# Kernel tuning notes

Measured on AMD Instinct MI355X. Metric: run time of the kernel, lower is better.

The kernel has to match this reference:

```python
import jax, jax.numpy as jnp
import numpy as np

HIDDEN_DIM = 64
VOCAB_SIZE = 64
NUM_SLOTS = 64
B, L = 256, 4096
EPS = 1e-5


def setup_inputs() -> dict:
    key = jax.random.key(0)
    ks = jax.random.split(key, 8)
    s = 0.02
    return {
        "seq": jax.random.randint(ks[0], (B, L), 0, VOCAB_SIZE),
        "embed": jax.random.normal(ks[1], (VOCAB_SIZE, HIDDEN_DIM), jnp.float32) * s,
        "W1": jax.random.normal(ks[2], (HIDDEN_DIM, 2 * HIDDEN_DIM), jnp.float32) * s,
        "b1": jnp.zeros((2 * HIDDEN_DIM,), jnp.float32),
        "W2": jax.random.normal(ks[3], (2 * HIDDEN_DIM, HIDDEN_DIM), jnp.float32) * s,
        "b2": jnp.zeros((HIDDEN_DIM,), jnp.float32),
        "gamma": jnp.ones((HIDDEN_DIM,), jnp.float32),
        "beta": jnp.zeros((HIDDEN_DIM,), jnp.float32),
        "Wq": jax.random.normal(ks[4], (HIDDEN_DIM, HIDDEN_DIM), jnp.float32) * s,
        "bq": jnp.zeros((HIDDEN_DIM,), jnp.float32),
        "Wo": jax.random.normal(ks[5], (HIDDEN_DIM, VOCAB_SIZE), jnp.float32) * s,
        "bo": jnp.zeros((VOCAB_SIZE,), jnp.float32),
    }


def reference(seq, embed, W1, b1, W2, b2, gamma, beta, Wq, bq, Wo, bo):
    # Encoder: embed -> FF residual -> LayerNorm
    e = embed[seq]                                   # [B, L, H]
    ff = jax.nn.relu(e @ W1 + b1) @ W2 + b2          # [B, L, H]
    h = e + ff
    mu = jnp.mean(h, axis=-1, keepdims=True)
    var = jnp.mean(jnp.square(h - mu), axis=-1, keepdims=True)
    hs = (h - mu) * jax.lax.rsqrt(var + EPS) * gamma + beta  # [B, L, H]

    # Top-k gating over content token norms
    content = hs[:, :-3, :]                          # [B, L-3, H]
    gate_scores = jnp.linalg.norm(content, axis=-1)  # [B, L-3]
    _, idx = jax.lax.top_k(gate_scores, NUM_SLOTS)   # [B, k], k == num_slots (L-3 >= k)
    slots = jnp.take_along_axis(content, idx[:, :, None], axis=1)  # [B, k, H]

    # Tiny single-query attention over gathered slots
    q = hs[:, -1, :] @ Wq + bq                       # [B, H]
    scores = jnp.einsum("bh,bkh->bk", q, slots) / jnp.sqrt(jnp.float32(HIDDEN_DIM))
    attn = jax.nn.softmax(scores, axis=-1)           # [B, k]
    ctx = jnp.einsum("bk,bkh->bh", attn, slots)      # [B, H]
    return ctx @ Wo + bo                             # [B, VOCAB]
```

## Files before the change

kernel.cpp:

```cpp
#include <hip/hip_runtime.h>
#include <math.h>

#define EPS 1e-5f

__global__ __launch_bounds__(256) void build_table(
    const float* __restrict__ embed,
    const float* __restrict__ W1, const float* __restrict__ b1,
    const float* __restrict__ W2, const float* __restrict__ b2,
    const float* __restrict__ gamma, const float* __restrict__ beta,
    float* __restrict__ wsf)
{
    __shared__ float W1s[64][128];
    __shared__ float W2s[128][64];
    __shared__ float e[64];
    __shared__ float Up[2][128];
    __shared__ float U[128];
    __shared__ float Hp[4][64];

    const int tid = threadIdx.x;
    const int t   = blockIdx.x;

    #pragma unroll
    for (int i = 0; i < 8; ++i) {
        reinterpret_cast<float4*>(&W1s[0][0])[tid + 256 * i] =
            reinterpret_cast<const float4*>(W1)[tid + 256 * i];
        reinterpret_cast<float4*>(&W2s[0][0])[tid + 256 * i] =
            reinterpret_cast<const float4*>(W2)[tid + 256 * i];
    }
    if (tid < 64) e[tid] = embed[t * 64 + tid];
    __syncthreads();

    {
        int j = tid & 127, h = tid >> 7;
        int k0 = h << 5;
        float acc = 0.f;
        #pragma unroll 8
        for (int k = 0; k < 32; ++k)
            acc = fmaf(e[k0 + k], W1s[k0 + k][j], acc);
        Up[h][j] = acc;
    }
    __syncthreads();
    if (tid < 128) U[tid] = fmaxf(b1[tid] + Up[0][tid] + Up[1][tid], 0.f);
    __syncthreads();

    {
        int j = tid & 63, qd = tid >> 6;
        int k0 = qd << 5;
        float acc = 0.f;
        #pragma unroll 8
        for (int k = 0; k < 32; ++k)
            acc = fmaf(U[k0 + k], W2s[k0 + k][j], acc);
        Hp[qd][j] = acc;
    }
    __syncthreads();

    if (tid < 64) {
        float h = e[tid] + b2[tid] + Hp[0][tid] + Hp[1][tid] + Hp[2][tid] + Hp[3][tid];
        float s = h;
        #pragma unroll
        for (int off = 1; off < 64; off <<= 1) s += __shfl_xor(s, off);
        float mu = s * (1.f / 64.f);
        float d = h - mu;
        float v = d * d;
        #pragma unroll
        for (int off = 1; off < 64; off <<= 1) v += __shfl_xor(v, off);
        float rstd = rsqrtf(v * (1.f / 64.f) + EPS);
        float hs = d * rstd * gamma[tid] + beta[tid];
        wsf[t * 64 + tid] = hs;
        float ss = hs * hs;
        #pragma unroll
        for (int off = 1; off < 64; off <<= 1) ss += __shfl_xor(ss, off);
        if (tid == 0) wsf[4096 + t] = sqrtf(ss);
    }
}

__global__ __launch_bounds__(256) void slot_epilogue(
    const int* __restrict__ seq,
    const float* __restrict__ Wq, const float* __restrict__ bq,
    const float* __restrict__ Wo, const float* __restrict__ bo,
    const float* __restrict__ wsf,
    float* __restrict__ out)
{
    __shared__ float HS[64][65];
    __shared__ int   hist[4][64];
    __shared__ float qv[64];
    __shared__ int   tlast_s;

    const int tid = threadIdx.x;
    const int wv  = tid >> 6;
    const int ln  = tid & 63;
    const int b   = blockIdx.x;
    const int* row = seq + b * 4096;

    hist[wv][ln] = 0;

    float wcol[64];
    float bias = 0.f, sc_r = 0.f;
    if (wv == 0) {
        #pragma unroll
        for (int k = 0; k < 64; ++k) wcol[k] = Wo[k * 64 + ln];
        bias = bo[ln];
        sc_r = wsf[4096 + ln];
    } else if (wv == 1) {
        #pragma unroll
        for (int k = 0; k < 64; ++k) wcol[k] = Wq[k * 64 + ln];
        bias = bq[ln];
    }

    #pragma unroll
    for (int i = 0; i < 4; ++i) {
        int idx4 = tid + 256 * i;
        float4 v = reinterpret_cast<const float4*>(wsf)[idx4];
        int t  = idx4 >> 4;
        int j0 = (idx4 & 15) << 2;
        HS[t][j0] = v.x; HS[t][j0 + 1] = v.y; HS[t][j0 + 2] = v.z; HS[t][j0 + 3] = v.w;
    }

    #pragma unroll
    for (int i = 0; i < 4; ++i) {
        int idx = tid + 256 * i;
        if (idx < 1023) {
            int4 v = reinterpret_cast<const int4*>(row)[idx];
            atomicAdd(&hist[wv][v.x], 1);
            atomicAdd(&hist[wv][v.y], 1);
            atomicAdd(&hist[wv][v.z], 1);
            atomicAdd(&hist[wv][v.w], 1);
        }
    }
    if (tid == 0) {
        atomicAdd(&hist[0][row[4092]], 1);
        tlast_s = row[4095];
    }
    __syncthreads();

    int cnt_i = 0;
    if (wv == 0) {
        int h = hist[0][ln] + hist[1][ln] + hist[2][ln] + hist[3][ln];
        float my = sc_r;
        int S = 0;
        for (int t2 = 0; t2 < 64; ++t2) {
            float s2 = __shfl(sc_r, t2);
            int   h2 = __shfl(h, t2);
            bool before = (s2 > my) || (s2 == my && t2 < ln);
            if (before) S += h2;
        }
        int rem = 64 - S;
        rem = rem < 0 ? 0 : rem;
        cnt_i = h < rem ? h : rem;
    } else if (wv == 1) {
        int tl = tlast_s;
        float acc = bias;
        #pragma unroll
        for (int k = 0; k < 64; ++k)
            acc = fmaf(HS[tl][k], wcol[k], acc);
        qv[ln] = acc;
    }
    __syncthreads();

    if (wv == 0) {
        float acc = 0.f;
        #pragma unroll 8
        for (int k = 0; k < 64; ++k)
            acc = fmaf(qv[k], HS[ln][k], acc);
        float logit = acc * 0.125f;
        float lm = (cnt_i > 0) ? logit : -1e30f;
        #pragma unroll
        for (int off = 1; off < 64; off <<= 1) lm = fmaxf(lm, __shfl_xor(lm, off));
        float wvv = (cnt_i > 0) ? (float)cnt_i * __expf(logit - lm) : 0.f;
        float z = wvv;
        #pragma unroll
        for (int off = 1; off < 64; off <<= 1) z += __shfl_xor(z, off);
        float w_reg = wvv / z;

        float cacc = 0.f;
        #pragma unroll 8
        for (int t2 = 0; t2 < 64; ++t2)
            cacc = fmaf(__shfl(w_reg, t2), HS[t2][ln], cacc);

        float oacc = bias;
        #pragma unroll
        for (int k = 0; k < 64; ++k)
            oacc = fmaf(__shfl(cacc, k), wcol[k], oacc);
        out[b * 64 + ln] = oacc;
    }
}

extern "C" void kernel_launch(void* const* d_in, const int* in_sizes, int n_in,
                              void* d_out, int out_size, void* d_ws, size_t ws_size,
                              hipStream_t stream) {
    const int*   seq   = (const int*)d_in[0];
    const float* embed = (const float*)d_in[1];
    const float* W1    = (const float*)d_in[2];
    const float* b1    = (const float*)d_in[3];
    const float* W2    = (const float*)d_in[4];
    const float* b2    = (const float*)d_in[5];
    const float* gamma = (const float*)d_in[6];
    const float* beta  = (const float*)d_in[7];
    const float* Wq    = (const float*)d_in[8];
    const float* bq    = (const float*)d_in[9];
    const float* Wo    = (const float*)d_in[10];
    const float* bo    = (const float*)d_in[11];
    float* out = (float*)d_out;
    float* wsf = (float*)d_ws;
    (void)in_sizes; (void)n_in; (void)out_size; (void)ws_size;

    build_table<<<64, 256, 0, stream>>>(embed, W1, b1, W2, b2, gamma, beta, wsf);
    slot_epilogue<<<256, 256, 0, stream>>>(seq, Wq, bq, Wo, bo, wsf, out);
}
```

Baseline: 16.98 us.

## Move per-row token histogram into first kernel to overlap with table build

The token histogram and last-token lookup over each sequence row now run in extra blocks of the first kernel, alongside the 64 table-building blocks, instead of inside the epilogue kernel. Per-row counts and the last-token index are written to workspace, and the epilogue only reads them. The aim is to hide the 4 MB sequence read behind the small table build, which uses few CUs, and to shorten the dependent second kernel. The cost is extra workspace traffic, plus one uniform launch that reserves the table path's large shared memory even in histogram blocks, which may reduce occupancy.

```diff
diff --git a/kernel.cpp b/kernel.cpp
--- a/kernel.cpp
+++ b/kernel.cpp
@@ -3,108 +3,141 @@
 
 #define EPS 1e-5f
 
-__global__ __launch_bounds__(256) void build_table(
+
+__global__ __launch_bounds__(256) void table_and_hist(
+    const int* __restrict__ seq,
     const float* __restrict__ embed,
     const float* __restrict__ W1, const float* __restrict__ b1,
     const float* __restrict__ W2, const float* __restrict__ b2,
     const float* __restrict__ gamma, const float* __restrict__ beta,
-    float* __restrict__ wsf)
+    float* __restrict__ wsf, int* __restrict__ wsi_hist,
+    int* __restrict__ wsi_tlast)
 {
-    __shared__ float W1s[64][128];
-    __shared__ float W2s[128][64];
-    __shared__ float e[64];
-    __shared__ float Up[2][128];
-    __shared__ float U[128];
-    __shared__ float Hp[4][64];
-
     const int tid = threadIdx.x;
-    const int t   = blockIdx.x;
-
-    #pragma unroll
-    for (int i = 0; i < 8; ++i) {
-        reinterpret_cast<float4*>(&W1s[0][0])[tid + 256 * i] =
-            reinterpret_cast<const float4*>(W1)[tid + 256 * i];
-        reinterpret_cast<float4*>(&W2s[0][0])[tid + 256 * i] =
-            reinterpret_cast<const float4*>(W2)[tid + 256 * i];
-    }
-    if (tid < 64) e[tid] = embed[t * 64 + tid];
-    __syncthreads();
-
-    {
-        int j = tid & 127, h = tid >> 7;
-        int k0 = h << 5;
-        float acc = 0.f;
-        #pragma unroll 8
-        for (int k = 0; k < 32; ++k)
-            acc = fmaf(e[k0 + k], W1s[k0 + k][j], acc);
-        Up[h][j] = acc;
-    }
-    __syncthreads();
-    if (tid < 128) U[tid] = fmaxf(b1[tid] + Up[0][tid] + Up[1][tid], 0.f);
-    __syncthreads();
-
-    {
-        int j = tid & 63, qd = tid >> 6;
-        int k0 = qd << 5;
-        float acc = 0.f;
-        #pragma unroll 8
-        for (int k = 0; k < 32; ++k)
-            acc = fmaf(U[k0 + k], W2s[k0 + k][j], acc);
-        Hp[qd][j] = acc;
-    }
-    __syncthreads();
-
-    if (tid < 64) {
-        float h = e[tid] + b2[tid] + Hp[0][tid] + Hp[1][tid] + Hp[2][tid] + Hp[3][tid];
-        float s = h;
-        #pragma unroll
-        for (int off = 1; off < 64; off <<= 1) s += __shfl_xor(s, off);
-        float mu = s * (1.f / 64.f);
-        float d = h - mu;
-        float v = d * d;
-        #pragma unroll
-        for (int off = 1; off < 64; off <<= 1) v += __shfl_xor(v, off);
-        float rstd = rsqrtf(v * (1.f / 64.f) + EPS);
-        float hs = d * rstd * gamma[tid] + beta[tid];
-        wsf[t * 64 + tid] = hs;
-        float ss = hs * hs;
-        #pragma unroll
-        for (int off = 1; off < 64; off <<= 1) ss += __shfl_xor(ss, off);
-        if (tid == 0) wsf[4096 + t] = sqrtf(ss);
+
+    if (blockIdx.x < 64) {
+        __shared__ float W1s[64][128];
+        __shared__ float W2s[128][64];
+        __shared__ float e[64];
+        __shared__ float Up[2][128];
+        __shared__ float U[128];
+        __shared__ float Hp[4][64];
+
+        const int t = blockIdx.x;
+
+        #pragma unroll
+        for (int i = 0; i < 8; ++i) {
+            reinterpret_cast<float4*>(&W1s[0][0])[tid + 256 * i] =
+                reinterpret_cast<const float4*>(W1)[tid + 256 * i];
+            reinterpret_cast<float4*>(&W2s[0][0])[tid + 256 * i] =
+                reinterpret_cast<const float4*>(W2)[tid + 256 * i];
+        }
+        if (tid < 64) e[tid] = embed[t * 64 + tid];
+        __syncthreads();
+
+        {
+            int j = tid & 127, h = tid >> 7;
+            int k0 = h << 5;
+            float acc = 0.f;
+            #pragma unroll 8
+            for (int k = 0; k < 32; ++k)
+                acc = fmaf(e[k0 + k], W1s[k0 + k][j], acc);
+            Up[h][j] = acc;
+        }
+        __syncthreads();
+        if (tid < 128) U[tid] = fmaxf(b1[tid] + Up[0][tid] + Up[1][tid], 0.f);
+        __syncthreads();
+
+        {
+            int j = tid & 63, qd = tid >> 6;
+            int k0 = qd << 5;
+            float acc = 0.f;
+            #pragma unroll 8
+            for (int k = 0; k < 32; ++k)
+                acc = fmaf(U[k0 + k], W2s[k0 + k][j], acc);
+            Hp[qd][j] = acc;
+        }
+        __syncthreads();
+
+        if (tid < 64) {
+            float h = e[tid] + b2[tid] + Hp[0][tid] + Hp[1][tid] + Hp[2][tid] + Hp[3][tid];
+            float s = h;
+            #pragma unroll
+            for (int off = 1; off < 64; off <<= 1) s += __shfl_xor(s, off);
+            float mu = s * (1.f / 64.f);
+            float d = h - mu;
+            float v = d * d;
+            #pragma unroll
+            for (int off = 1; off < 64; off <<= 1) v += __shfl_xor(v, off);
+            float rstd = rsqrtf(v * (1.f / 64.f) + EPS);
+            float hs = d * rstd * gamma[tid] + beta[tid];
+            wsf[t * 64 + tid] = hs;
+            float ss = hs * hs;
+            #pragma unroll
+            for (int off = 1; off < 64; off <<= 1) ss += __shfl_xor(ss, off);
+            if (tid == 0) wsf[4096 + t] = sqrtf(ss);
+        }
+    } else {
+        __shared__ int hist[4][64];
+        const int b = blockIdx.x - 64;
+        const int wv = tid >> 6, ln = tid & 63;
+        const int* row = seq + b * 4096;
+
+        hist[wv][ln] = 0;
+        __syncthreads();
+
+        #pragma unroll
+        for (int i = 0; i < 4; ++i) {
+            int idx = tid + 256 * i;
+            if (idx < 1023) {
+                int4 v = reinterpret_cast<const int4*>(row)[idx];
+                atomicAdd(&hist[wv][v.x], 1);
+                atomicAdd(&hist[wv][v.y], 1);
+                atomicAdd(&hist[wv][v.z], 1);
+                atomicAdd(&hist[wv][v.w], 1);
+            }
+        }
+        if (tid == 0) {
+            atomicAdd(&hist[0][row[4092]], 1);
+            wsi_tlast[b] = row[4095];
+        }
+        __syncthreads();
+
+        if (tid < 64)
+            wsi_hist[b * 64 + tid] =
+                hist[0][tid] + hist[1][tid] + hist[2][tid] + hist[3][tid];
     }
 }
 
 __global__ __launch_bounds__(256) void slot_epilogue(
-    const int* __restrict__ seq,
     const float* __restrict__ Wq, const float* __restrict__ bq,
     const float* __restrict__ Wo, const float* __restrict__ bo,
-    const float* __restrict__ wsf,
+    const float* __restrict__ wsf, const int* __restrict__ wsi_hist,
+    const int* __restrict__ wsi_tlast,
     float* __restrict__ out)
 {
     __shared__ float HS[64][65];
-    __shared__ int   hist[4][64];
     __shared__ float qv[64];
-    __shared__ int   tlast_s;
 
     const int tid = threadIdx.x;
     const int wv  = tid >> 6;
     const int ln  = tid & 63;
     const int b   = blockIdx.x;
-    const int* row = seq + b * 4096;
-
-    hist[wv][ln] = 0;
 
     float wcol[64];
     float bias = 0.f, sc_r = 0.f;
+    int h = 0, tl = 0;
     if (wv == 0) {
         #pragma unroll
         for (int k = 0; k < 64; ++k) wcol[k] = Wo[k * 64 + ln];
         bias = bo[ln];
         sc_r = wsf[4096 + ln];
+        h    = wsi_hist[b * 64 + ln];
     } else if (wv == 1) {
         #pragma unroll
         for (int k = 0; k < 64; ++k) wcol[k] = Wq[k * 64 + ln];
         bias = bq[ln];
+        tl   = wsi_tlast[b];
     }
 
     #pragma unroll
@@ -113,29 +146,12 @@
         float4 v = reinterpret_cast<const float4*>(wsf)[idx4];
         int t  = idx4 >> 4;
         int j0 = (idx4 & 15) << 2;
-        HS[t][j0] = v.x; HS[t][j0 + 1] = v.y; HS[t][j0 + 2] = v.z; HS[t][j0 + 3] = v.w;
-    }
-
-    #pragma unroll
-    for (int i = 0; i < 4; ++i) {
-        int idx = tid + 256 * i;
-        if (idx < 1023) {
-            int4 v = reinterpret_cast<const int4*>(row)[idx];
-            atomicAdd(&hist[wv][v.x], 1);
-            atomicAdd(&hist[wv][v.y], 1);
-            atomicAdd(&hist[wv][v.z], 1);
-            atomicAdd(&hist[wv][v.w], 1);
-        }
-    }
-    if (tid == 0) {
-        atomicAdd(&hist[0][row[4092]], 1);
-        tlast_s = row[4095];
+        HS[t][j0] = v.x; HS[t][j0+1] = v.y; HS[t][j0+2] = v.z; HS[t][j0+3] = v.w;
     }
     __syncthreads();
 
     int cnt_i = 0;
     if (wv == 0) {
-        int h = hist[0][ln] + hist[1][ln] + hist[2][ln] + hist[3][ln];
         float my = sc_r;
         int S = 0;
         for (int t2 = 0; t2 < 64; ++t2) {
@@ -148,7 +164,6 @@
         rem = rem < 0 ? 0 : rem;
         cnt_i = h < rem ? h : rem;
     } else if (wv == 1) {
-        int tl = tlast_s;
         float acc = bias;
         #pragma unroll
         for (int k = 0; k < 64; ++k)
@@ -202,8 +217,12 @@
     const float* bo    = (const float*)d_in[11];
     float* out = (float*)d_out;
     float* wsf = (float*)d_ws;
+    int*   wsi_hist  = (int*)(wsf + 4160);
+    int*   wsi_tlast = wsi_hist + 256 * 64;
     (void)in_sizes; (void)n_in; (void)out_size; (void)ws_size;
 
-    build_table<<<64, 256, 0, stream>>>(embed, W1, b1, W2, b2, gamma, beta, wsf);
-    slot_epilogue<<<256, 256, 0, stream>>>(seq, Wq, bq, Wo, bo, wsf, out);
+    table_and_hist<<<320, 256, 0, stream>>>(seq, embed, W1, b1, W2, b2,
+                                            gamma, beta, wsf, wsi_hist, wsi_tlast);
+    slot_epilogue<<<256, 256, 0, stream>>>(Wq, bq, Wo, bo, wsf, wsi_hist,
+                                           wsi_tlast, out);
 }
```

Result: no change. 16.94 us (-0.2%).

## Fuse table build and slot epilogue into one kernel with a global flag barrier

Applied to the files above, without the earlier changes.

Merges the two launches into a single kernel. The first 64 blocks compute the per-token LayerNorm table, publish it and increment a global counter. All blocks build their token histogram while that happens, then spin on the flag before reading the table. Sequence loads are issued early so they overlap with weight loading, and the W1/W2 shared-memory staging is replaced by direct global reads. This removes one kernel launch and the gap between launches, but it adds a memset, relies on all 256 blocks being co-resident (launch_bounds(256,1)), and risks deadlock if they are not.

```diff
diff --git a/kernel.cpp b/kernel.cpp
--- a/kernel.cpp
+++ b/kernel.cpp
@@ -3,86 +3,23 @@
 
 #define EPS 1e-5f
 
-__global__ __launch_bounds__(256) void build_table(
+__global__ __launch_bounds__(256, 1) void slot_one(
+    const int* __restrict__ seq,
     const float* __restrict__ embed,
     const float* __restrict__ W1, const float* __restrict__ b1,
     const float* __restrict__ W2, const float* __restrict__ b2,
     const float* __restrict__ gamma, const float* __restrict__ beta,
-    float* __restrict__ wsf)
-{
-    __shared__ float W1s[64][128];
-    __shared__ float W2s[128][64];
-    __shared__ float e[64];
-    __shared__ float Up[2][128];
-    __shared__ float U[128];
-    __shared__ float Hp[4][64];
-
-    const int tid = threadIdx.x;
-    const int t   = blockIdx.x;
-
-    #pragma unroll
-    for (int i = 0; i < 8; ++i) {
-        reinterpret_cast<float4*>(&W1s[0][0])[tid + 256 * i] =
-            reinterpret_cast<const float4*>(W1)[tid + 256 * i];
-        reinterpret_cast<float4*>(&W2s[0][0])[tid + 256 * i] =
-            reinterpret_cast<const float4*>(W2)[tid + 256 * i];
-    }
-    if (tid < 64) e[tid] = embed[t * 64 + tid];
-    __syncthreads();
-
-    {
-        int j = tid & 127, h = tid >> 7;
-        int k0 = h << 5;
-        float acc = 0.f;
-        #pragma unroll 8
-        for (int k = 0; k < 32; ++k)
-            acc = fmaf(e[k0 + k], W1s[k0 + k][j], acc);
-        Up[h][j] = acc;
-    }
-    __syncthreads();
-    if (tid < 128) U[tid] = fmaxf(b1[tid] + Up[0][tid] + Up[1][tid], 0.f);
-    __syncthreads();
-
-    {
-        int j = tid & 63, qd = tid >> 6;
-        int k0 = qd << 5;
-        float acc = 0.f;
-        #pragma unroll 8
-        for (int k = 0; k < 32; ++k)
-            acc = fmaf(U[k0 + k], W2s[k0 + k][j], acc);
-        Hp[qd][j] = acc;
-    }
-    __syncthreads();
-
-    if (tid < 64) {
-        float h = e[tid] + b2[tid] + Hp[0][tid] + Hp[1][tid] + Hp[2][tid] + Hp[3][tid];
-        float s = h;
-        #pragma unroll
-        for (int off = 1; off < 64; off <<= 1) s += __shfl_xor(s, off);
-        float mu = s * (1.f / 64.f);
-        float d = h - mu;
-        float v = d * d;
-        #pragma unroll
-        for (int off = 1; off < 64; off <<= 1) v += __shfl_xor(v, off);
-        float rstd = rsqrtf(v * (1.f / 64.f) + EPS);
-        float hs = d * rstd * gamma[tid] + beta[tid];
-        wsf[t * 64 + tid] = hs;
-        float ss = hs * hs;
-        #pragma unroll
-        for (int off = 1; off < 64; off <<= 1) ss += __shfl_xor(ss, off);
-        if (tid == 0) wsf[4096 + t] = sqrtf(ss);
-    }
-}
-
-__global__ __launch_bounds__(256) void slot_epilogue(
-    const int* __restrict__ seq,
     const float* __restrict__ Wq, const float* __restrict__ bq,
     const float* __restrict__ Wo, const float* __restrict__ bo,
-    const float* __restrict__ wsf,
+    float* __restrict__ wsf, int* __restrict__ flag,
     float* __restrict__ out)
 {
     __shared__ float HS[64][65];
     __shared__ int   hist[4][64];
+    __shared__ float e[64];
+    __shared__ float Up[2][128];
+    __shared__ float Ux[128];
+    __shared__ float Hp[4][64];
     __shared__ float qv[64];
     __shared__ int   tlast_s;
 
@@ -94,43 +31,100 @@
 
     hist[wv][ln] = 0;
 
+    int4 s0 = reinterpret_cast<const int4*>(row)[tid];
+    int4 s1 = reinterpret_cast<const int4*>(row)[tid + 256];
+    int4 s2 = reinterpret_cast<const int4*>(row)[tid + 512];
+    int4 s3 = reinterpret_cast<const int4*>(row)[tid + 768];
+
     float wcol[64];
-    float bias = 0.f, sc_r = 0.f;
+    float bias = 0.f;
     if (wv == 0) {
         #pragma unroll
         for (int k = 0; k < 64; ++k) wcol[k] = Wo[k * 64 + ln];
         bias = bo[ln];
-        sc_r = wsf[4096 + ln];
     } else if (wv == 1) {
         #pragma unroll
         for (int k = 0; k < 64; ++k) wcol[k] = Wq[k * 64 + ln];
         bias = bq[ln];
     }
+
+    if (b < 64 && tid < 64) e[tid] = embed[b * 64 + tid];
+    __syncthreads();
+
+    if (b < 64) {
+        {
+            int j = tid & 127, h = tid >> 7, k0 = h << 5;
+            float acc = 0.f;
+            #pragma unroll
+            for (int k = 0; k < 32; ++k)
+                acc = fmaf(e[k0 + k], W1[(k0 + k) * 128 + j], acc);
+            Up[h][j] = acc;
+        }
+        __syncthreads();
+        if (tid < 128) Ux[tid] = fmaxf(b1[tid] + Up[0][tid] + Up[1][tid], 0.f);
+        __syncthreads();
+        {
+            int j = tid & 63, qd = tid >> 6, k0 = qd << 5;
+            float acc = 0.f;
+            #pragma unroll
+            for (int k = 0; k < 32; ++k)
+                acc = fmaf(Ux[k0 + k], W2[(k0 + k) * 64 + j], acc);
+            Hp[qd][j] = acc;
+        }
+        __syncthreads();
+        if (tid < 64) {
+            float h = e[tid] + b2[tid] + Hp[0][tid] + Hp[1][tid] + Hp[2][tid] + Hp[3][tid];
+            float s = h;
+            #pragma unroll
+            for (int off = 1; off < 64; off <<= 1) s += __shfl_xor(s, off);
+            float mu = s * (1.f / 64.f);
+            float d = h - mu;
+            float v = d * d;
+            #pragma unroll
+            for (int off = 1; off < 64; off <<= 1) v += __shfl_xor(v, off);
+            float rstd = rsqrtf(v * (1.f / 64.f) + EPS);
+            float hs = d * rstd * gamma[tid] + beta[tid];
+            wsf[b * 64 + tid] = hs;
+            float ss = hs * hs;
+            #pragma unroll
+            for (int off = 1; off < 64; off <<= 1) ss += __shfl_xor(ss, off);
+            if (tid == 0) wsf[4096 + b] = sqrtf(ss);
+        }
+        __syncthreads();
+        __threadfence();
+        if (tid == 0) atomicAdd(flag, 1);
+    }
+
+    atomicAdd(&hist[wv][s0.x], 1); atomicAdd(&hist[wv][s0.y], 1);
+    atomicAdd(&hist[wv][s0.z], 1); atomicAdd(&hist[wv][s0.w], 1);
+    atomicAdd(&hist[wv][s1.x], 1); atomicAdd(&hist[wv][s1.y], 1);
+    atomicAdd(&hist[wv][s1.z], 1); atomicAdd(&hist[wv][s1.w], 1);
+    atomicAdd(&hist[wv][s2.x], 1); atomicAdd(&hist[wv][s2.y], 1);
+    atomicAdd(&hist[wv][s2.z], 1); atomicAdd(&hist[wv][s2.w], 1);
+    atomicAdd(&hist[wv][s3.x], 1);
+    if (tid != 255) {
+        atomicAdd(&hist[wv][s3.y], 1);
+        atomicAdd(&hist[wv][s3.z], 1);
+        atomicAdd(&hist[wv][s3.w], 1);
+    } else {
+        tlast_s = s3.w;
+    }
+    __syncthreads();
+
+    if (tid == 0) {
+        while (atomicAdd(flag, 0) < 64) __builtin_amdgcn_s_sleep(2);
+    }
+    __syncthreads();
+    __threadfence();
 
     #pragma unroll
     for (int i = 0; i < 4; ++i) {
         int idx4 = tid + 256 * i;
         float4 v = reinterpret_cast<const float4*>(wsf)[idx4];
-        int t  = idx4 >> 4;
-        int j0 = (idx4 & 15) << 2;
-        HS[t][j0] = v.x; HS[t][j0 + 1] = v.y; HS[t][j0 + 2] = v.z; HS[t][j0 + 3] = v.w;
-    }
-
-    #pragma unroll
-    for (int i = 0; i < 4; ++i) {
-        int idx = tid + 256 * i;
-        if (idx < 1023) {
-            int4 v = reinterpret_cast<const int4*>(row)[idx];
-            atomicAdd(&hist[wv][v.x], 1);
-            atomicAdd(&hist[wv][v.y], 1);
-            atomicAdd(&hist[wv][v.z], 1);
-            atomicAdd(&hist[wv][v.w], 1);
-        }
-    }
-    if (tid == 0) {
-        atomicAdd(&hist[0][row[4092]], 1);
-        tlast_s = row[4095];
-    }
+        int t = idx4 >> 4, j0 = (idx4 & 15) << 2;
+        HS[t][j0] = v.x; HS[t][j0+1] = v.y; HS[t][j0+2] = v.z; HS[t][j0+3] = v.w;
+    }
+    float sc_r = (wv == 0) ? wsf[4096 + ln] : 0.f;
     __syncthreads();
 
     int cnt_i = 0;
@@ -202,8 +196,10 @@
     const float* bo    = (const float*)d_in[11];
     float* out = (float*)d_out;
     float* wsf = (float*)d_ws;
+    int*   flag = (int*)(wsf + 4160);
     (void)in_sizes; (void)n_in; (void)out_size; (void)ws_size;
 
-    build_table<<<64, 256, 0, stream>>>(embed, W1, b1, W2, b2, gamma, beta, wsf);
-    slot_epilogue<<<256, 256, 0, stream>>>(seq, Wq, bq, Wo, bo, wsf, out);
+    hipMemsetAsync(flag, 0, sizeof(int), stream);
+    slot_one<<<256, 256, 0, stream>>>(seq, embed, W1, b1, W2, b2, gamma, beta,
+                                      Wq, bq, Wo, bo, wsf, flag, out);
 }
```

Result: slower. 41.80 us (+146.2%).

## Fuse table build into per-row kernel, recomputing vocab table in each block

Applied to the files above, without the earlier changes.

Replaces the two-kernel pipeline (build a 64-token normalized table, then per-row slot/attention epilogue) with a single kernel launched with 512 threads per row. Each block recomputes the full 64x64 embed->FF->LayerNorm table itself using register-tiled matmuls from shared memory, overlapping the sequence histogram load with that work. This removes one kernel launch and the inter-kernel dependency through workspace, at the cost of redundant table computation in all 256 blocks and much larger shared memory use per block.

```diff
diff --git a/kernel.cpp b/kernel.cpp
--- a/kernel.cpp
+++ b/kernel.cpp
@@ -3,87 +3,24 @@
 
 #define EPS 1e-5f
 
-__global__ __launch_bounds__(256) void build_table(
+__global__ __launch_bounds__(512, 1) void slot_single(
+    const int* __restrict__ seq,
     const float* __restrict__ embed,
     const float* __restrict__ W1, const float* __restrict__ b1,
     const float* __restrict__ W2, const float* __restrict__ b2,
     const float* __restrict__ gamma, const float* __restrict__ beta,
-    float* __restrict__ wsf)
+    const float* __restrict__ Wq, const float* __restrict__ bq,
+    const float* __restrict__ Wo, const float* __restrict__ bo,
+    float* __restrict__ out)
 {
+    __shared__ float Et[64][65];
     __shared__ float W1s[64][128];
     __shared__ float W2s[128][64];
-    __shared__ float e[64];
-    __shared__ float Up[2][128];
-    __shared__ float U[128];
-    __shared__ float Hp[4][64];
-
-    const int tid = threadIdx.x;
-    const int t   = blockIdx.x;
-
-    #pragma unroll
-    for (int i = 0; i < 8; ++i) {
-        reinterpret_cast<float4*>(&W1s[0][0])[tid + 256 * i] =
-            reinterpret_cast<const float4*>(W1)[tid + 256 * i];
-        reinterpret_cast<float4*>(&W2s[0][0])[tid + 256 * i] =
-            reinterpret_cast<const float4*>(W2)[tid + 256 * i];
-    }
-    if (tid < 64) e[tid] = embed[t * 64 + tid];
-    __syncthreads();
-
-    {
-        int j = tid & 127, h = tid >> 7;
-        int k0 = h << 5;
-        float acc = 0.f;
-        #pragma unroll 8
-        for (int k = 0; k < 32; ++k)
-            acc = fmaf(e[k0 + k], W1s[k0 + k][j], acc);
-        Up[h][j] = acc;
-    }
-    __syncthreads();
-    if (tid < 128) U[tid] = fmaxf(b1[tid] + Up[0][tid] + Up[1][tid], 0.f);
-    __syncthreads();
-
-    {
-        int j = tid & 63, qd = tid >> 6;
-        int k0 = qd << 5;
-        float acc = 0.f;
-        #pragma unroll 8
-        for (int k = 0; k < 32; ++k)
-            acc = fmaf(U[k0 + k], W2s[k0 + k][j], acc);
-        Hp[qd][j] = acc;
-    }
-    __syncthreads();
-
-    if (tid < 64) {
-        float h = e[tid] + b2[tid] + Hp[0][tid] + Hp[1][tid] + Hp[2][tid] + Hp[3][tid];
-        float s = h;
-        #pragma unroll
-        for (int off = 1; off < 64; off <<= 1) s += __shfl_xor(s, off);
-        float mu = s * (1.f / 64.f);
-        float d = h - mu;
-        float v = d * d;
-        #pragma unroll
-        for (int off = 1; off < 64; off <<= 1) v += __shfl_xor(v, off);
-        float rstd = rsqrtf(v * (1.f / 64.f) + EPS);
-        float hs = d * rstd * gamma[tid] + beta[tid];
-        wsf[t * 64 + tid] = hs;
-        float ss = hs * hs;
-        #pragma unroll
-        for (int off = 1; off < 64; off <<= 1) ss += __shfl_xor(ss, off);
-        if (tid == 0) wsf[4096 + t] = sqrtf(ss);
-    }
-}
-
-__global__ __launch_bounds__(256) void slot_epilogue(
-    const int* __restrict__ seq,
-    const float* __restrict__ Wq, const float* __restrict__ bq,
-    const float* __restrict__ Wo, const float* __restrict__ bo,
-    const float* __restrict__ wsf,
-    float* __restrict__ out)
-{
+    __shared__ float Ut[128][65];
     __shared__ float HS[64][65];
-    __shared__ int   hist[4][64];
+    __shared__ float Pp[8][64];
     __shared__ float qv[64];
+    __shared__ int   hist[8][64];
     __shared__ int   tlast_s;
 
     const int tid = threadIdx.x;
@@ -94,13 +31,15 @@
 
     hist[wv][ln] = 0;
 
+    int4 sA = reinterpret_cast<const int4*>(row)[tid];
+    int4 sB = reinterpret_cast<const int4*>(row)[tid + 512];
+
     float wcol[64];
-    float bias = 0.f, sc_r = 0.f;
+    float bias = 0.f;
     if (wv == 0) {
         #pragma unroll
         for (int k = 0; k < 64; ++k) wcol[k] = Wo[k * 64 + ln];
         bias = bo[ln];
-        sc_r = wsf[4096 + ln];
     } else if (wv == 1) {
         #pragma unroll
         for (int k = 0; k < 64; ++k) wcol[k] = Wq[k * 64 + ln];
@@ -109,37 +48,128 @@
 
     #pragma unroll
     for (int i = 0; i < 4; ++i) {
-        int idx4 = tid + 256 * i;
-        float4 v = reinterpret_cast<const float4*>(wsf)[idx4];
-        int t  = idx4 >> 4;
-        int j0 = (idx4 & 15) << 2;
-        HS[t][j0] = v.x; HS[t][j0 + 1] = v.y; HS[t][j0 + 2] = v.z; HS[t][j0 + 3] = v.w;
-    }
-
+        reinterpret_cast<float4*>(&W1s[0][0])[tid + 512 * i] =
+            reinterpret_cast<const float4*>(W1)[tid + 512 * i];
+        reinterpret_cast<float4*>(&W2s[0][0])[tid + 512 * i] =
+            reinterpret_cast<const float4*>(W2)[tid + 512 * i];
+    }
     #pragma unroll
-    for (int i = 0; i < 4; ++i) {
-        int idx = tid + 256 * i;
-        if (idx < 1023) {
-            int4 v = reinterpret_cast<const int4*>(row)[idx];
-            atomicAdd(&hist[wv][v.x], 1);
-            atomicAdd(&hist[wv][v.y], 1);
-            atomicAdd(&hist[wv][v.z], 1);
-            atomicAdd(&hist[wv][v.w], 1);
-        }
-    }
-    if (tid == 0) {
-        atomicAdd(&hist[0][row[4092]], 1);
-        tlast_s = row[4095];
+    for (int j = 0; j < 2; ++j) {
+        int f4 = tid + 512 * j;
+        float4 v = reinterpret_cast<const float4*>(embed)[f4];
+        int t = f4 >> 4, k0 = (f4 & 15) << 2;
+        Et[k0][t] = v.x; Et[k0+1][t] = v.y; Et[k0+2][t] = v.z; Et[k0+3][t] = v.w;
+    }
+    __syncthreads();
+
+    {
+        const int c0 = wv << 4;
+        float acc[16];
+        #pragma unroll
+        for (int m = 0; m < 4; ++m) {
+            float4 bb = *reinterpret_cast<const float4*>(&b1[c0 + 4*m]);
+            acc[4*m] = bb.x; acc[4*m+1] = bb.y; acc[4*m+2] = bb.z; acc[4*m+3] = bb.w;
+        }
+        for (int k = 0; k < 64; ++k) {
+            float e = Et[k][ln];
+            #pragma unroll
+            for (int m = 0; m < 4; ++m) {
+                float4 w = *reinterpret_cast<const float4*>(&W1s[k][c0 + 4*m]);
+                acc[4*m]   = fmaf(e, w.x, acc[4*m]);
+                acc[4*m+1] = fmaf(e, w.y, acc[4*m+1]);
+                acc[4*m+2] = fmaf(e, w.z, acc[4*m+2]);
+                acc[4*m+3] = fmaf(e, w.w, acc[4*m+3]);
+            }
+        }
+        #pragma unroll
+        for (int i = 0; i < 16; ++i)
+            Ut[c0 + i][ln] = fmaxf(acc[i], 0.f);
+    }
+
+    atomicAdd(&hist[wv][sA.x], 1); atomicAdd(&hist[wv][sA.y], 1);
+    atomicAdd(&hist[wv][sA.z], 1); atomicAdd(&hist[wv][sA.w], 1);
+    atomicAdd(&hist[wv][sB.x], 1);
+    if (tid != 511) {
+        atomicAdd(&hist[wv][sB.y], 1);
+        atomicAdd(&hist[wv][sB.z], 1);
+        atomicAdd(&hist[wv][sB.w], 1);
+    } else {
+        tlast_s = sB.w;
+    }
+    __syncthreads();
+
+    float hacc[8];
+    {
+        const int j0 = wv << 3;
+        #pragma unroll
+        for (int m = 0; m < 2; ++m) {
+            float4 bb = *reinterpret_cast<const float4*>(&b2[j0 + 4*m]);
+            hacc[4*m] = bb.x; hacc[4*m+1] = bb.y; hacc[4*m+2] = bb.z; hacc[4*m+3] = bb.w;
+        }
+        for (int k = 0; k < 128; ++k) {
+            float u = Ut[k][ln];
+            #pragma unroll
+            for (int m = 0; m < 2; ++m) {
+                float4 w = *reinterpret_cast<const float4*>(&W2s[k][j0 + 4*m]);
+                hacc[4*m]   = fmaf(u, w.x, hacc[4*m]);
+                hacc[4*m+1] = fmaf(u, w.y, hacc[4*m+1]);
+                hacc[4*m+2] = fmaf(u, w.z, hacc[4*m+2]);
+                hacc[4*m+3] = fmaf(u, w.w, hacc[4*m+3]);
+            }
+        }
+        #pragma unroll
+        for (int i = 0; i < 8; ++i) hacc[i] += Et[j0 + i][ln];
+
+        float s8 = 0.f;
+        #pragma unroll
+        for (int i = 0; i < 8; ++i) s8 += hacc[i];
+        Pp[wv][ln] = s8;
+    }
+    __syncthreads();
+
+    float mu;
+    {
+        float s = 0.f;
+        #pragma unroll
+        for (int w = 0; w < 8; ++w) s += Pp[w][ln];
+        mu = s * (1.f / 64.f);
+        float v8 = 0.f;
+        #pragma unroll
+        for (int i = 0; i < 8; ++i) { float d = hacc[i] - mu; v8 = fmaf(d, d, v8); }
+        __syncthreads();
+        Pp[wv][ln] = v8;
+    }
+    __syncthreads();
+    {
+        const int j0 = wv << 3;
+        float v = 0.f;
+        #pragma unroll
+        for (int w = 0; w < 8; ++w) v += Pp[w][ln];
+        float rstd = rsqrtf(v * (1.f / 64.f) + EPS);
+        float4 g0 = *reinterpret_cast<const float4*>(&gamma[j0]);
+        float4 g1 = *reinterpret_cast<const float4*>(&gamma[j0 + 4]);
+        float4 be0 = *reinterpret_cast<const float4*>(&beta[j0]);
+        float4 be1 = *reinterpret_cast<const float4*>(&beta[j0 + 4]);
+        float gg[8] = {g0.x,g0.y,g0.z,g0.w,g1.x,g1.y,g1.z,g1.w};
+        float bb[8] = {be0.x,be0.y,be0.z,be0.w,be1.x,be1.y,be1.z,be1.w};
+        #pragma unroll
+        for (int i = 0; i < 8; ++i)
+            HS[ln][j0 + i] = (hacc[i] - mu) * rstd * gg[i] + bb[i];
     }
     __syncthreads();
 
     int cnt_i = 0;
     if (wv == 0) {
-        int h = hist[0][ln] + hist[1][ln] + hist[2][ln] + hist[3][ln];
-        float my = sc_r;
+        int h = 0;
+        #pragma unroll
+        for (int w = 0; w < 8; ++w) h += hist[w][ln];
+        float ss = 0.f;
+        #pragma unroll 8
+        for (int k = 0; k < 64; ++k) ss = fmaf(HS[ln][k], HS[ln][k], ss);
+        float my = sqrtf(ss);
         int S = 0;
         for (int t2 = 0; t2 < 64; ++t2) {
-            float s2 = __shfl(sc_r, t2);
+            float s2 = __shfl(my, t2);
             int   h2 = __shfl(h, t2);
             bool before = (s2 > my) || (s2 == my && t2 < ln);
             if (before) S += h2;
@@ -201,9 +231,8 @@
     const float* Wo    = (const float*)d_in[10];
     const float* bo    = (const float*)d_in[11];
     float* out = (float*)d_out;
-    float* wsf = (float*)d_ws;
-    (void)in_sizes; (void)n_in; (void)out_size; (void)ws_size;
-
-    build_table<<<64, 256, 0, stream>>>(embed, W1, b1, W2, b2, gamma, beta, wsf);
-    slot_epilogue<<<256, 256, 0, stream>>>(seq, Wq, bq, Wo, bo, wsf, out);
+    (void)in_sizes; (void)n_in; (void)out_size; (void)d_ws; (void)ws_size;
+
+    slot_single<<<256, 512, 0, stream>>>(seq, embed, W1, b1, W2, b2,
+                                         gamma, beta, Wq, bq, Wo, bo, out);
 }
```

Result: slower. 25.60 us (+50.8%).
